# Kernel optimization log

Hardware: AMD Instinct MI355X
Metric: run time of the kernel (lower is better)

## Reference

```python
import jax, jax.numpy as jnp
import numpy as np

N, M, D = 62, 512, 256  # parts, batch samples (P*K = 64*8), hidden dim
K_PER_ID = 8
MARGIN = 0.2


def setup_inputs() -> dict:
    key = jax.random.key(0)
    k1, = jax.random.split(key, 1)
    feature = jax.random.normal(k1, (N, M, D), dtype=jnp.float32)
    # P*K structured labels (uniform class sizes are REQUIRED by the original
    # masked_select(...).view(n, m, -1) reshape): 64 ids, 8 samples each,
    # identical label layout for every part row n.
    row = jnp.arange(M, dtype=jnp.int64) // K_PER_ID  # [M]
    label = jnp.tile(row[None, :], (N, 1))            # [N, M]
    return {"feature": feature, "label": label}


def _safe_sqrt(x):
    # sqrt(relu(x)) with a zero (finite) gradient at x <= 0, matching the
    # forward values of torch.sqrt(F.relu(x)) exactly.
    pos = x > 0
    return jnp.where(pos, jnp.sqrt(jnp.where(pos, x, 1.0)), 0.0)


def reference(feature, label):
    # feature: [n, m, d], label: [n, m]
    sq = jnp.sum(feature * feature, axis=2)                       # [n, m]
    gram = jnp.einsum('nmd,nkd->nmk', feature, feature)           # [n, m, m]
    d2 = sq[:, :, None] + sq[:, None, :] - 2.0 * gram             # [n, m, m]
    dist = _safe_sqrt(jnp.maximum(d2, 0.0))                       # [n, m, m]

    dist_mean = jnp.mean(dist, axis=(1, 2))                       # [n]

    pos_mask = label[:, :, None] == label[:, None, :]             # [n, m, m]
    # hard positive: max dist over same-label columns (incl. self)
    hard_hp = jnp.max(jnp.where(pos_mask, dist, -jnp.inf), axis=2)   # [n, m]
    # hard negative: min dist over different-label columns
    hard_hn = jnp.min(jnp.where(pos_mask, jnp.inf, dist), axis=2)    # [n, m]

    hard_loss = jax.nn.relu(MARGIN + hard_hp - hard_hn)           # [n, m]
    hard_loss_mean = jnp.mean(hard_loss, axis=1)                  # [n]
    return hard_loss_mean, dist_mean
```

## Files before the change

### kernel.cpp

```cpp
#include <hip/hip_runtime.h>

#define N_PARTS 62
#define M_SAMP  512
#define D_DIM   256
#define MARGIN  0.2f
#define ROWS    (N_PARTS * M_SAMP)
#define PART_ELEMS (M_SAMP * D_DIM)

typedef unsigned short ushort_t;
typedef __attribute__((ext_vector_type(8))) short bf16x8;
typedef __attribute__((ext_vector_type(4))) float f32x4;

__device__ __forceinline__ ushort_t bf16_rne(float f) {
    unsigned u = __float_as_uint(f);
    unsigned r = u + 0x7fffu + ((u >> 16) & 1u);
    return (ushort_t)(r >> 16);
}

__global__ __launch_bounds__(256) void prep_kernel(const float* __restrict__ feat,
                                                   ushort_t* __restrict__ Fb,
                                                   float* __restrict__ sq,
                                                   float* __restrict__ out) {
    const int gid  = blockIdx.x * 256 + threadIdx.x;
    const int lane = threadIdx.x & 63;
    const int row  = gid >> 6;
    const int part = row >> 9, rp = row & 511;
    const float4 v = ((const float4*)(feat + (size_t)row * D_DIM))[lane];
    ushort4 us;
    us.x = bf16_rne(v.x); us.y = bf16_rne(v.y);
    us.z = bf16_rne(v.z); us.w = bf16_rne(v.w);
    const float fx = __uint_as_float((unsigned)us.x << 16);
    const float fy = __uint_as_float((unsigned)us.y << 16);
    const float fz = __uint_as_float((unsigned)us.z << 16);
    const float fw = __uint_as_float((unsigned)us.w << 16);
    const int c  = lane >> 3;
    const int q  = (lane >> 1) & 3;
    const int g  = rp >> 4;
    const int fl = (rp & 15) | (q << 4);
    *(ushort4*)(Fb + (size_t)part * PART_ELEMS + ((size_t)(c * 32 + g) * 512)
                + fl * 8 + (lane & 1) * 4) = us;
    float ssum = fx * fx + fy * fy + fz * fz + fw * fw;
    #pragma unroll
    for (int off = 32; off > 0; off >>= 1) ssum += __shfl_xor(ssum, off);
    if (lane == 0) sq[row] = ssum;
    if (gid < 2 * N_PARTS) out[gid] = 0.0f;
}

__global__ __launch_bounds__(512, 4) void fused_triplet_kernel(const ushort_t* __restrict__ Fb,
                                                               const float* __restrict__ sq,
                                                               float* __restrict__ out) {
    const int id = blockIdx.x;
    const int n  = id & 63;
    const int rt = id >> 6;
    if (n >= N_PARTS) return;
    const int r0 = rt * 64;
    const int tid = threadIdx.x;
    const int wave = tid >> 6, lane = tid & 63;
    const ushort_t* F = Fb + (size_t)n * PART_ELEMS;
    const float* SQ = sq + n * M_SAMP;

    __shared__ float mrg[8][64][3];

    f32x4 acc[4][4] = {};

    #pragma unroll 2
    for (int c = 0; c < 8; ++c) {
        const ushort_t* base = F + (size_t)c * (32 * 512);
        bf16x8 af[4], bf[4];
        #pragma unroll
        for (int mi = 0; mi < 4; ++mi)
            af[mi] = *(const bf16x8*)(base + (size_t)(rt * 4 + mi) * 512 + lane * 8);
        #pragma unroll
        for (int ni = 0; ni < 4; ++ni)
            bf[ni] = *(const bf16x8*)(base + (size_t)(wave * 4 + ni) * 512 + lane * 8);
        #pragma unroll
        for (int mi = 0; mi < 4; ++mi)
            #pragma unroll
            for (int ni = 0; ni < 4; ++ni)
                acc[mi][ni] = __builtin_amdgcn_mfma_f32_16x16x32_bf16(
                    af[mi], bf[ni], acc[mi][ni], 0, 0, 0);
    }

    float sqc[4];
    #pragma unroll
    for (int ni = 0; ni < 4; ++ni)
        sqc[ni] = SQ[wave * 64 + ni * 16 + (lane & 15)];
    #pragma unroll
    for (int mi = 0; mi < 4; ++mi) {
        #pragma unroll
        for (int p = 0; p < 4; ++p) {
            const int rl = mi * 16 + (lane >> 4) * 4 + p;
            const int R  = r0 + rl;
            const float sr = SQ[R];
            float ds = 0.f, hp = 0.f, hn = 1e30f;
            #pragma unroll
            for (int ni = 0; ni < 4; ++ni) {
                const int C = wave * 64 + ni * 16 + (lane & 15);
                const float d2 = sr + sqc[ni] - 2.f * acc[mi][ni][p];
                const float d  = sqrtf(fmaxf(d2, 0.f));
                ds += d;
                if ((R >> 3) == (C >> 3)) hp = fmaxf(hp, d);
                else                      hn = fminf(hn, d);
            }
            #pragma unroll
            for (int off = 1; off < 16; off <<= 1) {
                ds += __shfl_xor(ds, off);
                hp = fmaxf(hp, __shfl_xor(hp, off));
                hn = fminf(hn, __shfl_xor(hn, off));
            }
            if ((lane & 15) == 0) {
                mrg[wave][rl][0] = hp;
                mrg[wave][rl][1] = hn;
                mrg[wave][rl][2] = ds;
            }
        }
    }
    __syncthreads();
    if (tid < 64) {
        float hp = 0.f, hn = 1e30f, bd = 0.f;
        #pragma unroll
        for (int w = 0; w < 8; ++w) {
            hp = fmaxf(hp, mrg[w][tid][0]);
            hn = fminf(hn, mrg[w][tid][1]);
            bd += mrg[w][tid][2];
        }
        float bl = fmaxf(MARGIN + hp - hn, 0.f);
        #pragma unroll
        for (int off = 32; off > 0; off >>= 1) {
            bl += __shfl_xor(bl, off);
            bd += __shfl_xor(bd, off);
        }
        if (lane == 0) {
            atomicAdd(&out[n],           bl * (1.0f / 512.0f));
            atomicAdd(&out[N_PARTS + n], bd * (1.0f / (512.0f * 512.0f)));
        }
    }
}

extern "C" void kernel_launch(void* const* d_in, const int* in_sizes, int n_in,
                              void* d_out, int out_size, void* d_ws, size_t ws_size,
                              hipStream_t stream) {
    const float* feat = (const float*)d_in[0];
    float* out = (float*)d_out;

    ushort_t* Fb = (ushort_t*)d_ws;
    float* sq    = (float*)((char*)d_ws + (size_t)ROWS * D_DIM * 2);

    prep_kernel<<<dim3(ROWS / 4), 256, 0, stream>>>(feat, Fb, sq, out);
    fused_triplet_kernel<<<dim3(512), 512, 0, stream>>>(Fb, sq, out);
}
```

Baseline: 99.50 us.

## Exploit distance symmetry: reduce per column to shrink shuffle reductions

Swaps the roles of rows and columns so each wave owns a 64-row slice and the block owns a 64-column tile. Because the distance matrix is symmetric, per-column reductions give the same per-sample hard positive, hard negative and distance sum. Each lane now accumulates 16 values in registers before a 2-step cross-lane shuffle, instead of a 4-step shuffle for every row, cutting shuffle and LDS-write work. It also fully unrolls the K loop and uses the raw hardware sqrt, trading a larger register footprint and slightly less precise sqrt.

```diff
diff --git a/kernel.cpp b/kernel.cpp
--- a/kernel.cpp
+++ b/kernel.cpp
@@ -51,9 +51,8 @@
                                                                float* __restrict__ out) {
     const int id = blockIdx.x;
     const int n  = id & 63;
-    const int rt = id >> 6;
+    const int ct = id >> 6;
     if (n >= N_PARTS) return;
-    const int r0 = rt * 64;
     const int tid = threadIdx.x;
     const int wave = tid >> 6, lane = tid & 63;
     const ushort_t* F = Fb + (size_t)n * PART_ELEMS;
@@ -63,16 +62,18 @@
 
     f32x4 acc[4][4] = {};
 
-    #pragma unroll 2
+    const ushort_t* aptr = F + (size_t)(wave * 4) * 512 + lane * 8;
+    const ushort_t* bptr = F + (size_t)(ct * 4) * 512 + lane * 8;
+
+    #pragma unroll
     for (int c = 0; c < 8; ++c) {
-        const ushort_t* base = F + (size_t)c * (32 * 512);
+        const size_t off = (size_t)c * (32 * 512);
         bf16x8 af[4], bf[4];
         #pragma unroll
-        for (int mi = 0; mi < 4; ++mi)
-            af[mi] = *(const bf16x8*)(base + (size_t)(rt * 4 + mi) * 512 + lane * 8);
-        #pragma unroll
-        for (int ni = 0; ni < 4; ++ni)
-            bf[ni] = *(const bf16x8*)(base + (size_t)(wave * 4 + ni) * 512 + lane * 8);
+        for (int i = 0; i < 4; ++i) {
+            af[i] = *(const bf16x8*)(aptr + off + (size_t)i * 512);
+            bf[i] = *(const bf16x8*)(bptr + off + (size_t)i * 512);
+        }
         #pragma unroll
         for (int mi = 0; mi < 4; ++mi)
             #pragma unroll
@@ -81,38 +82,41 @@
                     af[mi], bf[ni], acc[mi][ni], 0, 0, 0);
     }
 
-    float sqc[4];
+    float sqr[4][4];
     #pragma unroll
-    for (int ni = 0; ni < 4; ++ni)
-        sqc[ni] = SQ[wave * 64 + ni * 16 + (lane & 15)];
+    for (int mi = 0; mi < 4; ++mi)
+        #pragma unroll
+        for (int p = 0; p < 4; ++p)
+            sqr[mi][p] = SQ[wave * 64 + mi * 16 + (lane >> 4) * 4 + p];
+
     #pragma unroll
-    for (int mi = 0; mi < 4; ++mi) {
+    for (int ni = 0; ni < 4; ++ni) {
+        const int C = ct * 64 + ni * 16 + (lane & 15);
+        const float sc = SQ[C];
+        const int Cg = C >> 3;
+        float ds = 0.f, hp = 0.f, hn = 1e30f;
         #pragma unroll
-        for (int p = 0; p < 4; ++p) {
-            const int rl = mi * 16 + (lane >> 4) * 4 + p;
-            const int R  = r0 + rl;
-            const float sr = SQ[R];
-            float ds = 0.f, hp = 0.f, hn = 1e30f;
+        for (int mi = 0; mi < 4; ++mi) {
             #pragma unroll
-            for (int ni = 0; ni < 4; ++ni) {
-                const int C = wave * 64 + ni * 16 + (lane & 15);
-                const float d2 = sr + sqc[ni] - 2.f * acc[mi][ni][p];
-                const float d  = sqrtf(fmaxf(d2, 0.f));
+            for (int p = 0; p < 4; ++p) {
+                const int R = wave * 64 + mi * 16 + (lane >> 4) * 4 + p;
+                const float d2 = sqr[mi][p] + sc - 2.f * acc[mi][ni][p];
+                const float d  = __builtin_amdgcn_sqrtf(fmaxf(d2, 0.f));
                 ds += d;
-                if ((R >> 3) == (C >> 3)) hp = fmaxf(hp, d);
-                else                      hn = fminf(hn, d);
+                if ((R >> 3) == Cg) hp = fmaxf(hp, d);
+                else                hn = fminf(hn, d);
             }
-            #pragma unroll
-            for (int off = 1; off < 16; off <<= 1) {
-                ds += __shfl_xor(ds, off);
-                hp = fmaxf(hp, __shfl_xor(hp, off));
-                hn = fminf(hn, __shfl_xor(hn, off));
-            }
-            if ((lane & 15) == 0) {
-                mrg[wave][rl][0] = hp;
-                mrg[wave][rl][1] = hn;
-                mrg[wave][rl][2] = ds;
-            }
+        }
+        #pragma unroll
+        for (int off = 16; off < 64; off <<= 1) {
+            ds += __shfl_xor(ds, off);
+            hp = fmaxf(hp, __shfl_xor(hp, off));
+            hn = fminf(hn, __shfl_xor(hn, off));
+        }
+        if (lane < 16) {
+            mrg[wave][ni * 16 + lane][0] = hp;
+            mrg[wave][ni * 16 + lane][1] = hn;
+            mrg[wave][ni * 16 + lane][2] = ds;
         }
     }
     __syncthreads();
```

After: 92.92 us. -6.6%, faster.
